# Kernel optimization log

Measured on AMD Instinct MI355X. Metric: run time of the kernel, lower is better.

## Reference

```python
import jax, jax.numpy as jnp
import numpy as np

WS = 8        # window_size
SHIFT = True
NHEADS = 4
DIM = 192

def _ln(x, g, b, eps=1e-5):
    mu = jnp.mean(x, axis=-1, keepdims=True)
    var = jnp.var(x, axis=-1, keepdims=True)
    return (x - mu) * jax.lax.rsqrt(var + eps) * g + b

def setup_inputs() -> dict:
    key = jax.random.key(0)
    ks = jax.random.split(key, 16)
    d = DIM
    s = 0.02
    return {
        "x":      jax.random.normal(ks[0], (4, d, 256, 256), jnp.float32),
        "g1":     jnp.ones((d,), jnp.float32),
        "b1":     jnp.zeros((d,), jnp.float32),
        "w_qkv":  jax.random.normal(ks[1], (d, 3 * d), jnp.float32) * s,
        "b_qkv":  jnp.zeros((3 * d,), jnp.float32),
        "w_o":    jax.random.normal(ks[2], (d, d), jnp.float32) * s,
        "b_o":    jnp.zeros((d,), jnp.float32),
        "g2":     jnp.ones((d,), jnp.float32),
        "b2":     jnp.zeros((d,), jnp.float32),
        "w_m1":   jax.random.normal(ks[3], (d, 4 * d), jnp.float32) * s,
        "b_m1":   jnp.zeros((4 * d,), jnp.float32),
        "w_m2":   jax.random.normal(ks[4], (4 * d, d), jnp.float32) * s,
        "b_m2":   jnp.zeros((d,), jnp.float32),
    }

def reference(x, g1, b1, w_qkv, b_qkv, w_o, b_o, g2, b2, w_m1, b_m1, w_m2, b_m2):
    B, C, H, W = x.shape
    pad_h = (-H) % WS
    pad_w = (-W) % WS
    x = jnp.pad(x, ((0, 0), (0, 0), (0, pad_h), (0, pad_w)))
    Hp, Wp = H + pad_h, W + pad_w
    if SHIFT:
        x = jnp.roll(x, (-(WS // 2), -(WS // 2)), axis=(2, 3))
    # window partition: (B,C,Hp,Wp) -> (nW, WS*WS, C)
    w = x.reshape(B, C, Hp // WS, WS, Wp // WS, WS)
    w = jnp.transpose(w, (0, 2, 4, 3, 5, 1)).reshape(-1, WS * WS, C)
    w = _ln(w, g1, b1)
    # multi-head self-attention (torch MHA: fused qkv proj, scale 1/sqrt(hd))
    qkv = w @ w_qkv + b_qkv                      # (nW, T, 3C)
    q, k, v = jnp.split(qkv, 3, axis=-1)
    hd = C // NHEADS
    def heads(t):
        return t.reshape(t.shape[0], t.shape[1], NHEADS, hd).transpose(0, 2, 1, 3)
    q, k, v = heads(q), heads(k), heads(v)
    scale = 1.0 / np.sqrt(hd).astype(np.float32)
    attn = jax.nn.softmax(jnp.einsum('nhqd,nhkd->nhqk', q * scale, k), axis=-1)
    o = jnp.einsum('nhqk,nhkd->nhqd', attn, v)
    o = o.transpose(0, 2, 1, 3).reshape(-1, WS * WS, C) @ w_o + b_o
    w = w + o
    h = _ln(w, g2, b2)
    w = w + (jax.nn.gelu(h @ w_m1 + b_m1, approximate=False) @ w_m2 + b_m2)
    # window reverse: (nW, WS*WS, C) -> (B,C,Hp,Wp)
    x = w.reshape(B, Hp // WS, Wp // WS, WS, WS, C)
    x = jnp.transpose(x, (0, 5, 1, 3, 2, 4)).reshape(B, C, Hp, Wp)
    if SHIFT:
        x = jnp.roll(x, (WS // 2, WS // 2), axis=(2, 3))
    return x[:, :, :H, :W]
```

## Files before the change

### kernel.cpp

```cpp
#include <hip/hip_runtime.h>
#include <hip/hip_bf16.h>
#include <cmath>


using bf16 = __hip_bfloat16;
typedef __attribute__((ext_vector_type(8))) short short8;
typedef __attribute__((ext_vector_type(4))) float f32x4;

__device__ __forceinline__ float b2f(bf16 v) { return __bfloat162float(v); }
__device__ __forceinline__ bf16  f2b(float v) { return __float2bfloat16(v); }

template <bool ISBF>
__device__ __forceinline__ float gldf(const void* p, size_t i) {
  if constexpr (ISBF) return b2f(((const bf16*)p)[i]);
  else                return ((const float*)p)[i];
}
template <bool ISBF>
__device__ __forceinline__ void gst(void* p, size_t i, float v) {
  if constexpr (ISBF) ((bf16*)p)[i] = f2b(v);
  else                ((float*)p)[i] = v;
}

template <bool ISBF>
__device__ __forceinline__ void transpose_body(
    const void* w_qkv, const void* w_o, const void* w_m1, const void* w_m2,
    bf16* ws, int id)
{
  if (id < 110592) {
    int n = id / 192, k = id - n * 192;
    ws[id] = f2b(gldf<ISBF>(w_qkv, (size_t)k * 576 + n));
  } else if (id < 147456) {
    int l = id - 110592;
    int n = l / 192, k = l - n * 192;
    ws[id] = f2b(gldf<ISBF>(w_o, (size_t)k * 192 + n));
  } else if (id < 294912) {
    int l = id - 147456;
    int n = l / 192, k = l - n * 192;
    ws[id] = f2b(gldf<ISBF>(w_m1, (size_t)k * 768 + n));
  } else {
    int l = id - 294912;
    int n = l / 768, k = l - n * 768;
    ws[id] = f2b(gldf<ISBF>(w_m2, (size_t)k * 192 + n));
  }
}

__global__ __launch_bounds__(256) void transpose_weights(
    const void* w_qkv, const void* w_o, const void* w_m1, const void* w_m2,
    bf16* ws, int isbf)
{
  int id = blockIdx.x * 256 + threadIdx.x;
  if (id >= 442368) return;
  if (isbf) transpose_body<true >(w_qkv, w_o, w_m1, w_m2, ws, id);
  else      transpose_body<false>(w_qkv, w_o, w_m1, w_m2, ws, id);
}

__device__ __forceinline__ void stage48(bf16* dst, const bf16* src, int tid) {
  for (int idx = tid; idx < 1152; idx += 256) {
    int r = idx / 24, g = idx - r * 24;
    *reinterpret_cast<short8*>(dst + r * 200 + g * 8) =
        *reinterpret_cast<const short8*>(src + r * 192 + g * 8);
  }
}
__device__ __forceinline__ void stage96(bf16* dst, const bf16* srcBase,
                                        int srcStride, int kOff, int tid) {
  for (int i = 0; i < 3; ++i) {
    int idx = tid + i * 256;
    int r = idx >> 3, g = idx & 7;
    short8 v = {0, 0, 0, 0, 0, 0, 0, 0};
    if (g < 6)
      v = *reinterpret_cast<const short8*>(srcBase + (size_t)r * srcStride +
                                           kOff + g * 8);
    *reinterpret_cast<short8*>(dst + r * 72 + g * 8) = v;
  }
}

template <int NT, int KS>
__device__ __forceinline__ void gemm_tile(const bf16* sA, int lda,
                                          const bf16* sB, int ldb,
                                          f32x4* c, int w, int col, int quad) {
  const bf16* ap = sA + (w * 16 + col) * lda + quad * 8;
#pragma unroll
  for (int ks = 0; ks < KS; ++ks) {
    short8 a = *reinterpret_cast<const short8*>(ap + ks * 32);
#pragma unroll
    for (int nt = 0; nt < NT; ++nt) {
      short8 b = *reinterpret_cast<const short8*>(
          sB + (nt * 16 + col) * ldb + ks * 32 + quad * 8);
      c[nt] = __builtin_amdgcn_mfma_f32_16x16x32_bf16(a, b, c[nt], 0, 0, 0);
    }
  }
}

template <bool ISBF>
__device__ void swin_mfma_body(
    const void* __restrict__ x,
    const void* __restrict__ g1, const void* __restrict__ b1,
    const void* __restrict__ b_qkv, const void* __restrict__ b_o,
    const void* __restrict__ g2, const void* __restrict__ b2,
    const void* __restrict__ b_m1, const void* __restrict__ b_m2,
    const bf16* __restrict__ ws, void* __restrict__ out, char* smem)
{
  bf16* sX = reinterpret_cast<bf16*>(smem);
  bf16* sW = reinterpret_cast<bf16*>(smem + 25600);
  bf16* sQ = reinterpret_cast<bf16*>(smem + 44800);
  bf16* sK = reinterpret_cast<bf16*>(smem + 54016);
  bf16* sV = reinterpret_cast<bf16*>(smem + 63232);
  bf16* sP = reinterpret_cast<bf16*>(smem + 70144);
  float* red = reinterpret_cast<float*>(smem + 70144);

  const bf16* wsq  = ws;
  const bf16* wso  = ws + 110592;
  const bf16* wsm1 = ws + 147456;
  const bf16* wsm2 = ws + 294912;

  const int wi = blockIdx.x;
  const int bb = wi >> 10, hy = (wi >> 5) & 31, wx = wi & 31;
  const int tid = threadIdx.x;
  const int w = tid >> 6, lane = tid & 63, col = lane & 15, quad = lane >> 4;
  const int t = tid >> 2, qq = tid & 3;
  const int ty = t >> 3, tx = t & 7;
  const int ph = (hy * 8 + ty + 4) & 255;
  const int pw = (wx * 8 + tx + 4) & 255;

  {
    int buf = tid >> 7, rh = tid & 127, row = rh >> 1, half = rh & 1;
    short8 z = {0, 0, 0, 0, 0, 0, 0, 0};
    *reinterpret_cast<short8*>((buf ? sK : sQ) + row * 72 + 48 + half * 8) = z;
  }

  {
    const size_t xb = (((size_t)(bb * 192 + qq * 48)) << 16) + (ph << 8) + pw;
    float s = 0.f, ss = 0.f;
    for (int j = 0; j < 48; ++j) {
      float v = gldf<ISBF>(x, xb + ((size_t)j << 16));
      s += v; ss += v * v;
      sX[t * 200 + qq * 48 + j] = f2b(v);
    }
    red[(t * 4 + qq) * 2 + 0] = s;
    red[(t * 4 + qq) * 2 + 1] = ss;
  }
  __syncthreads();
  {
    float s = 0.f, ss = 0.f;
    for (int k = 0; k < 4; ++k) {
      s  += red[(t * 4 + k) * 2 + 0];
      ss += red[(t * 4 + k) * 2 + 1];
    }
    float mu  = s * (1.f / 192.f);
    float var = ss * (1.f / 192.f) - mu * mu;
    float inv = rsqrtf(var + 1e-5f);
    for (int j = 0; j < 48; ++j) {
      int c = qq * 48 + j;
      float v = b2f(sX[t * 200 + c]);
      sX[t * 200 + c] =
          f2b((v - mu) * inv * gldf<ISBF>(g1, c) + gldf<ISBF>(b1, c));
    }
  }

  f32x4 accW[12];
#pragma unroll
  for (int i = 0; i < 12; ++i) accW[i] = {0.f, 0.f, 0.f, 0.f};
  const float scale = 0.14433756729740643f;

  for (int h = 0; h < 4; ++h) {
    __syncthreads();
    stage48(sW, wsq + (size_t)(h * 48) * 192, tid);
    __syncthreads();
    {
      f32x4 c3[3] = {{0,0,0,0},{0,0,0,0},{0,0,0,0}};
      gemm_tile<3, 6>(sX, 200, sW, 200, c3, w, col, quad);
#pragma unroll
      for (int nt = 0; nt < 3; ++nt) {
        float bq = gldf<ISBF>(b_qkv, h * 48 + nt * 16 + col);
#pragma unroll
        for (int r = 0; r < 4; ++r)
          sQ[(w * 16 + quad * 4 + r) * 72 + nt * 16 + col] =
              f2b((c3[nt][r] + bq) * scale);
      }
    }
    __syncthreads();
    stage48(sW, wsq + (size_t)(192 + h * 48) * 192, tid);
    __syncthreads();
    {
      f32x4 c3[3] = {{0,0,0,0},{0,0,0,0},{0,0,0,0}};
      gemm_tile<3, 6>(sX, 200, sW, 200, c3, w, col, quad);
#pragma unroll
      for (int nt = 0; nt < 3; ++nt) {
        float bk = gldf<ISBF>(b_qkv, 192 + h * 48 + nt * 16 + col);
#pragma unroll
        for (int r = 0; r < 4; ++r)
          sK[(w * 16 + quad * 4 + r) * 72 + nt * 16 + col] = f2b(c3[nt][r] + bk);
      }
    }
    __syncthreads();
    stage48(sW, wsq + (size_t)(384 + h * 48) * 192, tid);
    __syncthreads();
    {
      f32x4 c3[3] = {{0,0,0,0},{0,0,0,0},{0,0,0,0}};
      gemm_tile<3, 6>(sX, 200, sW, 200, c3, w, col, quad);
#pragma unroll
      for (int nt = 0; nt < 3; ++nt) {
        float bv = gldf<ISBF>(b_qkv, 384 + h * 48 + nt * 16 + col);
#pragma unroll
        for (int r = 0; r < 4; ++r)
          sV[(nt * 16 + col) * 72 + w * 16 + quad * 4 + r] = f2b(c3[nt][r] + bv);
      }
    }
    __syncthreads();

    {
      f32x4 s4[4] = {{0,0,0,0},{0,0,0,0},{0,0,0,0},{0,0,0,0}};
      gemm_tile<4, 2>(sQ, 72, sK, 72, s4, w, col, quad);
      float inv[4];
#pragma unroll
      for (int r = 0; r < 4; ++r) {
        float m = fmaxf(fmaxf(s4[0][r], s4[1][r]), fmaxf(s4[2][r], s4[3][r]));
#pragma unroll
        for (int msk = 1; msk < 16; msk <<= 1) m = fmaxf(m, __shfl_xor(m, msk, 64));
        float sum = 0.f;
#pragma unroll
        for (int nt = 0; nt < 4; ++nt) {
          float e = expf(s4[nt][r] - m);
          s4[nt][r] = e; sum += e;
        }
#pragma unroll
        for (int msk = 1; msk < 16; msk <<= 1) sum += __shfl_xor(sum, msk, 64);
        inv[r] = 1.f / sum;
      }
#pragma unroll
      for (int nt = 0; nt < 4; ++nt)
#pragma unroll
        for (int r = 0; r < 4; ++r)
          sP[(w * 16 + quad * 4 + r) * 72 + nt * 16 + col] =
              f2b(s4[nt][r] * inv[r]);
    }
    {
      f32x4 c3[3] = {{0,0,0,0},{0,0,0,0},{0,0,0,0}};
      gemm_tile<3, 2>(sP, 72, sV, 72, c3, w, col, quad);
#pragma unroll
      for (int nt = 0; nt < 3; ++nt)
#pragma unroll
        for (int r = 0; r < 4; ++r)
          sQ[(w * 16 + quad * 4 + r) * 72 + nt * 16 + col] = f2b(c3[nt][r]);
    }
    for (int s = 0; s < 2; ++s) {
      __syncthreads();
      stage96(sW, wso + (size_t)(s * 96) * 192, 192, h * 48, tid);
      __syncthreads();
      gemm_tile<6, 2>(sQ, 72, sW, 72, accW + s * 6, w, col, quad);
    }
  }

  {
#pragma unroll
    for (int nt = 0; nt < 12; ++nt) {
      int c = nt * 16 + col;
      float bo = gldf<ISBF>(b_o, c);
#pragma unroll
      for (int r = 0; r < 4; ++r)
        accW[nt][r] += bo + b2f(sX[(w * 16 + quad * 4 + r) * 200 + c]);
    }
    float su[4] = {0,0,0,0}, sq[4] = {0,0,0,0};
#pragma unroll
    for (int nt = 0; nt < 12; ++nt)
#pragma unroll
      for (int r = 0; r < 4; ++r) {
        su[r] += accW[nt][r]; sq[r] += accW[nt][r] * accW[nt][r];
      }
#pragma unroll
    for (int r = 0; r < 4; ++r) {
#pragma unroll
      for (int msk = 1; msk < 16; msk <<= 1) {
        su[r] += __shfl_xor(su[r], msk, 64);
        sq[r] += __shfl_xor(sq[r], msk, 64);
      }
    }
    float mu[4], inv[4];
#pragma unroll
    for (int r = 0; r < 4; ++r) {
      mu[r] = su[r] * (1.f / 192.f);
      inv[r] = rsqrtf(sq[r] * (1.f / 192.f) - mu[r] * mu[r] + 1e-5f);
    }
#pragma unroll
    for (int nt = 0; nt < 12; ++nt) {
      int c = nt * 16 + col;
      float g2c = gldf<ISBF>(g2, c), b2c = gldf<ISBF>(b2, c);
      float bm2 = gldf<ISBF>(b_m2, c);
#pragma unroll
      for (int r = 0; r < 4; ++r) {
        float hv = (accW[nt][r] - mu[r]) * inv[r] * g2c + b2c;
        sX[(w * 16 + quad * 4 + r) * 200 + c] = f2b(hv);
        accW[nt][r] += bm2;
      }
    }
  }

  for (int ch = 0; ch < 16; ++ch) {
    __syncthreads();
    stage48(sW, wsm1 + (size_t)(ch * 48) * 192, tid);
    __syncthreads();
    {
      f32x4 c3[3] = {{0,0,0,0},{0,0,0,0},{0,0,0,0}};
      gemm_tile<3, 6>(sX, 200, sW, 200, c3, w, col, quad);
#pragma unroll
      for (int nt = 0; nt < 3; ++nt) {
        float bm1 = gldf<ISBF>(b_m1, ch * 48 + nt * 16 + col);
#pragma unroll
        for (int r = 0; r < 4; ++r) {
          float v = c3[nt][r] + bm1;
          v = 0.5f * v * (1.f + erff(v * 0.70710678118654752f));
          sK[(w * 16 + quad * 4 + r) * 72 + nt * 16 + col] = f2b(v);
        }
      }
    }
    for (int s = 0; s < 2; ++s) {
      __syncthreads();
      stage96(sW, wsm2 + (size_t)(s * 96) * 768, 768, ch * 48, tid);
      __syncthreads();
      gemm_tile<6, 2>(sK, 72, sW, 72, accW + s * 6, w, col, quad);
    }
  }

  __syncthreads();
#pragma unroll
  for (int nt = 0; nt < 12; ++nt)
#pragma unroll
    for (int r = 0; r < 4; ++r)
      sX[(w * 16 + quad * 4 + r) * 200 + nt * 16 + col] = f2b(accW[nt][r]);
  __syncthreads();
  {
    const size_t ob = (((size_t)(bb * 192 + qq * 48)) << 16) + (ph << 8) + pw;
    for (int j = 0; j < 48; ++j)
      gst<ISBF>(out, ob + ((size_t)j << 16), b2f(sX[t * 200 + qq * 48 + j]));
  }
}

__global__ __launch_bounds__(256, 2) void swin_mfma(
    const void* x, const void* g1, const void* b1, const void* b_qkv,
    const void* b_o, const void* g2, const void* b2, const void* b_m1,
    const void* b_m2, const bf16* ws, void* out, int isbf)
{
  __shared__ __align__(16) char smem[79360];
  if (isbf)
    swin_mfma_body<true >(x, g1, b1, b_qkv, b_o, g2, b2, b_m1, b_m2, ws, out, smem);
  else
    swin_mfma_body<false>(x, g1, b1, b_qkv, b_o, g2, b2, b_m1, b_m2, ws, out, smem);
}

template <bool ISBF>
__device__ __forceinline__ void gld4(const void* p, size_t i, float* o) {
  if constexpr (ISBF) {
    uint2 u = *reinterpret_cast<const uint2*>((const bf16*)p + i);
    union { unsigned int b; float f; } a;
    a.b = u.x << 16;          o[0] = a.f;
    a.b = u.x & 0xffff0000u;  o[1] = a.f;
    a.b = u.y << 16;          o[2] = a.f;
    a.b = u.y & 0xffff0000u;  o[3] = a.f;
  } else {
    float4 f = *reinterpret_cast<const float4*>((const float*)p + i);
    o[0] = f.x; o[1] = f.y; o[2] = f.z; o[3] = f.w;
  }
}

template <bool ISBF>
__device__ void swin_scalar_body(
    const void* x, const void* g1, const void* b1, const void* w_qkv,
    const void* b_qkv, const void* w_o, const void* b_o, const void* g2,
    const void* b2, const void* w_m1, const void* b_m1, const void* w_m2,
    const void* b_m2, void* out, bf16* s_w, char* s_buf)
{
  bf16*  sQ  = reinterpret_cast<bf16*>(s_buf);
  bf16*  sK  = reinterpret_cast<bf16*>(s_buf + 6400);
  bf16*  sV  = reinterpret_cast<bf16*>(s_buf + 12800);
  float* sS  = reinterpret_cast<float*>(s_buf + 19200);
  bf16*  sO  = sQ;
  bf16*  sH  = reinterpret_cast<bf16*>(s_buf);
  bf16*  sC  = reinterpret_cast<bf16*>(s_buf + 25600);
  float* red1 = reinterpret_cast<float*>(s_buf);
  float* red2 = reinterpret_cast<float*>(s_buf + 25600);

  const int wi = blockIdx.x;
  const int bb = wi >> 10, hy = (wi >> 5) & 31, wx = wi & 31;
  const int tid = threadIdx.x;
  const int t = tid >> 2, q = tid & 3;
  const int ty = t >> 3, tx = t & 7;
  const int ph = (hy * 8 + ty + 4) & 255, pw = (wx * 8 + tx + 4) & 255;
  float acc[48];
  {
    const size_t xb = (((size_t)(bb * 192 + q * 48)) << 16) + (ph << 8) + pw;
    float s = 0.f, ss = 0.f;
    for (int j = 0; j < 48; ++j) {
      float v = gldf<ISBF>(x, xb + ((size_t)j << 16));
      s += v; ss += v * v;
      s_w[t * 200 + q * 48 + j] = f2b(v);
    }
    red1[(t * 4 + q) * 2 + 0] = s; red1[(t * 4 + q) * 2 + 1] = ss;
  }
  __syncthreads();
  {
    float s = 0.f, ss = 0.f;
    for (int k = 0; k < 4; ++k) { s += red1[(t*4+k)*2]; ss += red1[(t*4+k)*2+1]; }
    float mu = s / 192.f, var = ss / 192.f - mu * mu, inv = rsqrtf(var + 1e-5f);
    for (int j = 0; j < 48; ++j) {
      int c = q * 48 + j;
      float v = (b2f(s_w[t*200+c]) - mu) * inv * gldf<ISBF>(g1,c) + gldf<ISBF>(b1,c);
      s_w[t * 200 + c] = f2b(v);
      acc[j] = v;
    }
  }
  __syncthreads();
  const float scale = 0.14433756729740643f;
  for (int h = 0; h < 4; ++h) {
    {
      float aq[12], ak[12], av[12];
      for (int j = 0; j < 12; ++j) {
        aq[j] = gldf<ISBF>(b_qkv, h*48 + q*12 + j);
        ak[j] = gldf<ISBF>(b_qkv, 192 + h*48 + q*12 + j);
        av[j] = gldf<ISBF>(b_qkv, 384 + h*48 + q*12 + j);
      }
      for (int c = 0; c < 192; ++c) {
        float a = b2f(s_w[t * 200 + c]);
        const size_t wr = (size_t)c * 576 + h * 48 + q * 12;
        float wv[4];
        for (int j0 = 0; j0 < 12; j0 += 4) {
          gld4<ISBF>(w_qkv, wr + j0, wv);
          for (int k = 0; k < 4; ++k) aq[j0+k] += a * wv[k];
        }
        for (int j0 = 0; j0 < 12; j0 += 4) {
          gld4<ISBF>(w_qkv, wr + 192 + j0, wv);
          for (int k = 0; k < 4; ++k) ak[j0+k] += a * wv[k];
        }
        for (int j0 = 0; j0 < 12; j0 += 4) {
          gld4<ISBF>(w_qkv, wr + 384 + j0, wv);
          for (int k = 0; k < 4; ++k) av[j0+k] += a * wv[k];
        }
      }
      for (int j = 0; j < 12; ++j) {
        sQ[t*50 + q*12 + j] = f2b(aq[j] * scale);
        sK[t*50 + q*12 + j] = f2b(ak[j]);
        sV[t*50 + q*12 + j] = f2b(av[j]);
      }
    }
    __syncthreads();
    {
      float as[16];
      for (int j = 0; j < 16; ++j) as[j] = 0.f;
      for (int d = 0; d < 48; ++d) {
        float qv = b2f(sQ[t*50 + d]);
        for (int j = 0; j < 16; ++j) as[j] += qv * b2f(sK[(q*16+j)*50 + d]);
      }
      for (int j = 0; j < 16; ++j) sS[t*66 + q*16 + j] = as[j];
    }
    __syncthreads();
    if (tid < 64) {
      float mx = -1e30f;
      for (int j = 0; j < 64; ++j) mx = fmaxf(mx, sS[tid*66+j]);
      float sum = 0.f;
      for (int j = 0; j < 64; ++j) { float e = expf(sS[tid*66+j]-mx); sS[tid*66+j]=e; sum+=e; }
      float r = 1.f / sum;
      for (int j = 0; j < 64; ++j) sS[tid*66+j] *= r;
    }
    __syncthreads();
    {
      float ao[12];
      for (int j = 0; j < 12; ++j) ao[j] = 0.f;
      for (int j = 0; j < 64; ++j) {
        float p = sS[t*66 + j];
        for (int k = 0; k < 12; ++k) ao[k] += p * b2f(sV[j*50 + q*12 + k]);
      }
      for (int j = 0; j < 12; ++j) sO[t*50 + q*12 + j] = f2b(ao[j]);
    }
    __syncthreads();
    for (int d = 0; d < 48; ++d) {
      float ov = b2f(sO[t*50 + d]);
      const size_t wr = (size_t)(h*48+d) * 192 + q * 48;
      float wv[4];
      for (int j0 = 0; j0 < 48; j0 += 4) {
        gld4<ISBF>(w_o, wr + j0, wv);
        for (int k = 0; k < 4; ++k) acc[j0+k] += ov * wv[k];
      }
    }
    __syncthreads();
  }
  for (int j = 0; j < 48; ++j) acc[j] += gldf<ISBF>(b_o, q*48 + j);
  {
    float s = 0.f, ss = 0.f;
    for (int j = 0; j < 48; ++j) { s += acc[j]; ss += acc[j]*acc[j]; }
    red2[(t*4+q)*2] = s; red2[(t*4+q)*2+1] = ss;
  }
  __syncthreads();
  {
    float s = 0.f, ss = 0.f;
    for (int k = 0; k < 4; ++k) { s += red2[(t*4+k)*2]; ss += red2[(t*4+k)*2+1]; }
    float mu = s/192.f, var = ss/192.f - mu*mu, inv = rsqrtf(var + 1e-5f);
    for (int j = 0; j < 48; ++j) {
      int c = q*48 + j;
      sH[t*200+c] = f2b((acc[j]-mu)*inv*gldf<ISBF>(g2,c) + gldf<ISBF>(b2,c));
    }
  }
  for (int j = 0; j < 48; ++j) acc[j] += gldf<ISBF>(b_m2, q*48 + j);
  __syncthreads();
  for (int ch = 0; ch < 8; ++ch) {
    float am[24];
    for (int j = 0; j < 24; ++j) am[j] = gldf<ISBF>(b_m1, ch*96 + q*24 + j);
    for (int c = 0; c < 192; ++c) {
      float hv = b2f(sH[t*200 + c]);
      const size_t wr = (size_t)c * 768 + ch*96 + q*24;
      float wv[4];
      for (int j0 = 0; j0 < 24; j0 += 4) {
        gld4<ISBF>(w_m1, wr + j0, wv);
        for (int k = 0; k < 4; ++k) am[j0+k] += hv * wv[k];
      }
    }
    for (int j = 0; j < 24; ++j) {
      float v = am[j];
      am[j] = 0.5f * v * (1.f + erff(v * 0.70710678118654752f));
    }
    for (int j = 0; j < 24; ++j) sC[t*104 + q*24 + j] = f2b(am[j]);
    __syncthreads();
    for (int u = 0; u < 96; ++u) {
      float hv = b2f(sC[t*104 + u]);
      const size_t wr = (size_t)(ch*96+u) * 192 + q*48;
      float wv[4];
      for (int j0 = 0; j0 < 48; j0 += 4) {
        gld4<ISBF>(w_m2, wr + j0, wv);
        for (int k = 0; k < 4; ++k) acc[j0+k] += hv * wv[k];
      }
    }
    __syncthreads();
  }
  {
    const size_t ob = (((size_t)(bb*192 + q*48)) << 16) + (ph << 8) + pw;
    for (int j = 0; j < 48; ++j) gst<ISBF>(out, ob + ((size_t)j << 16), acc[j]);
  }
}

__global__ __launch_bounds__(256) void swin_scalar(
    const void* x, const void* g1, const void* b1, const void* w_qkv,
    const void* b_qkv, const void* w_o, const void* b_o, const void* g2,
    const void* b2, const void* w_m1, const void* b_m1, const void* w_m2,
    const void* b_m2, void* out, int isbf)
{
  __shared__ bf16 s_w[64 * 200];
  __shared__ __align__(16) char s_buf[38912];
  if (isbf)
    swin_scalar_body<true >(x,g1,b1,w_qkv,b_qkv,w_o,b_o,g2,b2,w_m1,b_m1,w_m2,b_m2,out,s_w,s_buf);
  else
    swin_scalar_body<false>(x,g1,b1,w_qkv,b_qkv,w_o,b_o,g2,b2,w_m1,b_m1,w_m2,b_m2,out,s_w,s_buf);
}

extern "C" void kernel_launch(void* const* d_in, const int* in_sizes, int n_in,
                              void* d_out, int out_size, void* d_ws, size_t ws_size,
                              hipStream_t stream) {
  const int isbf = (n_in > 1 && in_sizes != nullptr && in_sizes[1] == 384) ? 1 : 0;
  if (ws_size >= 884736) {
    transpose_weights<<<dim3(1728), dim3(256), 0, stream>>>(
        d_in[3], d_in[5], d_in[9], d_in[11], (bf16*)d_ws, isbf);
    swin_mfma<<<dim3(4096), dim3(256), 0, stream>>>(
        d_in[0], d_in[1], d_in[2], d_in[4], d_in[6], d_in[7], d_in[8],
        d_in[10], d_in[12], (const bf16*)d_ws, d_out, isbf);
  } else {
    swin_scalar<<<dim3(4096), dim3(256), 0, stream>>>(
        d_in[0], d_in[1], d_in[2], d_in[3], d_in[4], d_in[5], d_in[6],
        d_in[7], d_in[8], d_in[9], d_in[10], d_in[11], d_in[12], d_out, isbf);
  }
}
```

Baseline: 1.470 ms.

## Read MFMA weight fragments directly from global memory instead of LDS staging

Drops the stage48/stage96 LDS staging of weight tiles. Each GEMM now loads its B fragments straight from the pre-transposed global weight buffer, which should be cache-resident. This removes many block-wide barriers and LDS copies, and shrinks shared memory from about 79KB to 60KB. In exchange, each of the four waves fetches the same weight fragments separately from global memory, so MFMA issue is exposed to L1/L2 latency and extra cache traffic.

```diff
diff --git a/kernel.cpp b/kernel.cpp
--- a/kernel.cpp
+++ b/kernel.cpp
@@ -54,26 +54,6 @@
   else      transpose_body<false>(w_qkv, w_o, w_m1, w_m2, ws, id);
 }
 
-__device__ __forceinline__ void stage48(bf16* dst, const bf16* src, int tid) {
-  for (int idx = tid; idx < 1152; idx += 256) {
-    int r = idx / 24, g = idx - r * 24;
-    *reinterpret_cast<short8*>(dst + r * 200 + g * 8) =
-        *reinterpret_cast<const short8*>(src + r * 192 + g * 8);
-  }
-}
-__device__ __forceinline__ void stage96(bf16* dst, const bf16* srcBase,
-                                        int srcStride, int kOff, int tid) {
-  for (int i = 0; i < 3; ++i) {
-    int idx = tid + i * 256;
-    int r = idx >> 3, g = idx & 7;
-    short8 v = {0, 0, 0, 0, 0, 0, 0, 0};
-    if (g < 6)
-      v = *reinterpret_cast<const short8*>(srcBase + (size_t)r * srcStride +
-                                           kOff + g * 8);
-    *reinterpret_cast<short8*>(dst + r * 72 + g * 8) = v;
-  }
-}
-
 template <int NT, int KS>
 __device__ __forceinline__ void gemm_tile(const bf16* sA, int lda,
                                           const bf16* sB, int ldb,
@@ -86,6 +66,40 @@
     for (int nt = 0; nt < NT; ++nt) {
       short8 b = *reinterpret_cast<const short8*>(
           sB + (nt * 16 + col) * ldb + ks * 32 + quad * 8);
+      c[nt] = __builtin_amdgcn_mfma_f32_16x16x32_bf16(a, b, c[nt], 0, 0, 0);
+    }
+  }
+}
+
+template <int NT, int KS>
+__device__ __forceinline__ void gemm_gB(const bf16* sA, int lda,
+    const bf16* __restrict__ gB, int ldk, f32x4* c, int w, int col, int quad) {
+  const bf16* ap = sA + (w * 16 + col) * lda + quad * 8;
+  const bf16* bp = gB + col * ldk + quad * 8;
+#pragma unroll
+  for (int ks = 0; ks < KS; ++ks) {
+    short8 a = *reinterpret_cast<const short8*>(ap + ks * 32);
+#pragma unroll
+    for (int nt = 0; nt < NT; ++nt) {
+      short8 b = *reinterpret_cast<const short8*>(bp + nt * 16 * ldk + ks * 32);
+      c[nt] = __builtin_amdgcn_mfma_f32_16x16x32_bf16(a, b, c[nt], 0, 0, 0);
+    }
+  }
+}
+
+template <int NT>
+__device__ __forceinline__ void gemm_gB_p48(const bf16* sA, int lda,
+    const bf16* __restrict__ gB, int ldk, f32x4* c, int w, int col, int quad) {
+  const bf16* ap = sA + (w * 16 + col) * lda + quad * 8;
+  const bf16* bp = gB + col * ldk + quad * 8;
+#pragma unroll
+  for (int ks = 0; ks < 2; ++ks) {
+    short8 a = *reinterpret_cast<const short8*>(ap + ks * 32);
+#pragma unroll
+    for (int nt = 0; nt < NT; ++nt) {
+      short8 b = {0, 0, 0, 0, 0, 0, 0, 0};
+      if (ks == 0 || quad < 2)
+        b = *reinterpret_cast<const short8*>(bp + nt * 16 * ldk + ks * 32);
       c[nt] = __builtin_amdgcn_mfma_f32_16x16x32_bf16(a, b, c[nt], 0, 0, 0);
     }
   }
@@ -101,12 +115,11 @@
     const bf16* __restrict__ ws, void* __restrict__ out, char* smem)
 {
   bf16* sX = reinterpret_cast<bf16*>(smem);
-  bf16* sW = reinterpret_cast<bf16*>(smem + 25600);
-  bf16* sQ = reinterpret_cast<bf16*>(smem + 44800);
-  bf16* sK = reinterpret_cast<bf16*>(smem + 54016);
-  bf16* sV = reinterpret_cast<bf16*>(smem + 63232);
-  bf16* sP = reinterpret_cast<bf16*>(smem + 70144);
-  float* red = reinterpret_cast<float*>(smem + 70144);
+  bf16* sQ = reinterpret_cast<bf16*>(smem + 25600);
+  bf16* sK = reinterpret_cast<bf16*>(smem + 34816);
+  bf16* sV = reinterpret_cast<bf16*>(smem + 44032);
+  bf16* sP = reinterpret_cast<bf16*>(smem + 50944);
+  float* red = reinterpret_cast<float*>(smem + 50944);
 
   const bf16* wsq  = ws;
   const bf16* wso  = ws + 110592;
@@ -156,6 +169,7 @@
           f2b((v - mu) * inv * gldf<ISBF>(g1, c) + gldf<ISBF>(b1, c));
     }
   }
+  __syncthreads();
 
   f32x4 accW[12];
 #pragma unroll
@@ -163,12 +177,10 @@
   const float scale = 0.14433756729740643f;
 
   for (int h = 0; h < 4; ++h) {
-    __syncthreads();
-    stage48(sW, wsq + (size_t)(h * 48) * 192, tid);
-    __syncthreads();
+    if (h) __syncthreads();
     {
       f32x4 c3[3] = {{0,0,0,0},{0,0,0,0},{0,0,0,0}};
-      gemm_tile<3, 6>(sX, 200, sW, 200, c3, w, col, quad);
+      gemm_gB<3, 6>(sX, 200, wsq + (size_t)(h * 48) * 192, 192, c3, w, col, quad);
 #pragma unroll
       for (int nt = 0; nt < 3; ++nt) {
         float bq = gldf<ISBF>(b_qkv, h * 48 + nt * 16 + col);
@@ -178,12 +190,9 @@
               f2b((c3[nt][r] + bq) * scale);
       }
     }
-    __syncthreads();
-    stage48(sW, wsq + (size_t)(192 + h * 48) * 192, tid);
-    __syncthreads();
     {
       f32x4 c3[3] = {{0,0,0,0},{0,0,0,0},{0,0,0,0}};
-      gemm_tile<3, 6>(sX, 200, sW, 200, c3, w, col, quad);
+      gemm_gB<3, 6>(sX, 200, wsq + (size_t)(192 + h * 48) * 192, 192, c3, w, col, quad);
 #pragma unroll
       for (int nt = 0; nt < 3; ++nt) {
         float bk = gldf<ISBF>(b_qkv, 192 + h * 48 + nt * 16 + col);
@@ -192,12 +201,9 @@
           sK[(w * 16 + quad * 4 + r) * 72 + nt * 16 + col] = f2b(c3[nt][r] + bk);
       }
     }
-    __syncthreads();
-    stage48(sW, wsq + (size_t)(384 + h * 48) * 192, tid);
-    __syncthreads();
     {
       f32x4 c3[3] = {{0,0,0,0},{0,0,0,0},{0,0,0,0}};
-      gemm_tile<3, 6>(sX, 200, sW, 200, c3, w, col, quad);
+      gemm_gB<3, 6>(sX, 200, wsq + (size_t)(384 + h * 48) * 192, 192, c3, w, col, quad);
 #pragma unroll
       for (int nt = 0; nt < 3; ++nt) {
         float bv = gldf<ISBF>(b_qkv, 384 + h * 48 + nt * 16 + col);
@@ -234,6 +240,8 @@
           sP[(w * 16 + quad * 4 + r) * 72 + nt * 16 + col] =
               f2b(s4[nt][r] * inv[r]);
     }
+    __syncthreads();
+
     {
       f32x4 c3[3] = {{0,0,0,0},{0,0,0,0},{0,0,0,0}};
       gemm_tile<3, 2>(sP, 72, sV, 72, c3, w, col, quad);
@@ -243,13 +251,14 @@
         for (int r = 0; r < 4; ++r)
           sQ[(w * 16 + quad * 4 + r) * 72 + nt * 16 + col] = f2b(c3[nt][r]);
     }
-    for (int s = 0; s < 2; ++s) {
-      __syncthreads();
-      stage96(sW, wso + (size_t)(s * 96) * 192, 192, h * 48, tid);
-      __syncthreads();
-      gemm_tile<6, 2>(sQ, 72, sW, 72, accW + s * 6, w, col, quad);
-    }
-  }
+    __syncthreads();
+
+    gemm_gB_p48<6>(sQ, 72, wso + (size_t)(0 * 96) * 192 + h * 48, 192,
+                   accW + 0, w, col, quad);
+    gemm_gB_p48<6>(sQ, 72, wso + (size_t)(1 * 96) * 192 + h * 48, 192,
+                   accW + 6, w, col, quad);
+  }
+  __syncthreads();
 
   {
 #pragma unroll
@@ -294,14 +303,12 @@
       }
     }
   }
+  __syncthreads();
 
   for (int ch = 0; ch < 16; ++ch) {
-    __syncthreads();
-    stage48(sW, wsm1 + (size_t)(ch * 48) * 192, tid);
-    __syncthreads();
     {
       f32x4 c3[3] = {{0,0,0,0},{0,0,0,0},{0,0,0,0}};
-      gemm_tile<3, 6>(sX, 200, sW, 200, c3, w, col, quad);
+      gemm_gB<3, 6>(sX, 200, wsm1 + (size_t)(ch * 48) * 192, 192, c3, w, col, quad);
 #pragma unroll
       for (int nt = 0; nt < 3; ++nt) {
         float bm1 = gldf<ISBF>(b_m1, ch * 48 + nt * 16 + col);
@@ -313,12 +320,11 @@
         }
       }
     }
-    for (int s = 0; s < 2; ++s) {
-      __syncthreads();
-      stage96(sW, wsm2 + (size_t)(s * 96) * 768, 768, ch * 48, tid);
-      __syncthreads();
-      gemm_tile<6, 2>(sK, 72, sW, 72, accW + s * 6, w, col, quad);
-    }
+    __syncthreads();
+    gemm_gB_p48<6>(sK, 72, wsm2 + (size_t)(0 * 96) * 768 + ch * 48, 768,
+                   accW + 0, w, col, quad);
+    gemm_gB_p48<6>(sK, 72, wsm2 + (size_t)(1 * 96) * 768 + ch * 48, 768,
+                   accW + 6, w, col, quad);
   }
 
   __syncthreads();
@@ -340,7 +346,7 @@
     const void* b_o, const void* g2, const void* b2, const void* b_m1,
     const void* b_m2, const bf16* ws, void* out, int isbf)
 {
-  __shared__ __align__(16) char smem[79360];
+  __shared__ __align__(16) char smem[60160];
   if (isbf)
     swin_mfma_body<true >(x, g1, b1, b_qkv, b_o, g2, b2, b_m1, b_m2, ws, out, smem);
   else
```

Measured after the change: 2.158 ms. 1.47x slower.

## Process two windows per block sharing staged weight tiles in LDS

Applied to the files above, without the earlier changes.

Each 512-thread block now handles two windows. One shared weight staging buffer serves both windows, and each window keeps its own activation, Q/K/V and P buffers. The aim is to halve the global-to-LDS weight traffic per window and the number of staging passes. In exchange LDS use per block grows to about 122KB, so only one block fits per CU, and barriers now synchronize all 512 threads.

```diff
diff --git a/kernel.cpp b/kernel.cpp
--- a/kernel.cpp
+++ b/kernel.cpp
@@ -54,23 +54,27 @@
   else      transpose_body<false>(w_qkv, w_o, w_m1, w_m2, ws, id);
 }
 
-__device__ __forceinline__ void stage48(bf16* dst, const bf16* src, int tid) {
-  for (int idx = tid; idx < 1152; idx += 256) {
+__device__ __forceinline__ void stage48_512(bf16* dst, const bf16* src,
+                                            int tid512) {
+  for (int idx = tid512; idx < 1152; idx += 512) {
     int r = idx / 24, g = idx - r * 24;
     *reinterpret_cast<short8*>(dst + r * 200 + g * 8) =
         *reinterpret_cast<const short8*>(src + r * 192 + g * 8);
   }
 }
-__device__ __forceinline__ void stage96(bf16* dst, const bf16* srcBase,
-                                        int srcStride, int kOff, int tid) {
-  for (int i = 0; i < 3; ++i) {
-    int idx = tid + i * 256;
-    int r = idx >> 3, g = idx & 7;
-    short8 v = {0, 0, 0, 0, 0, 0, 0, 0};
-    if (g < 6)
-      v = *reinterpret_cast<const short8*>(srcBase + (size_t)r * srcStride +
-                                           kOff + g * 8);
-    *reinterpret_cast<short8*>(dst + r * 72 + g * 8) = v;
+__device__ __forceinline__ void stage96_512(bf16* dst, const bf16* srcBase,
+                                            int srcStride, int kOff,
+                                            int tid512) {
+  for (int i = 0; i < 2; ++i) {
+    int idx = tid512 + i * 512;
+    if (idx < 768) {
+      int r = idx >> 3, g = idx & 7;
+      short8 v = {0, 0, 0, 0, 0, 0, 0, 0};
+      if (g < 6)
+        v = *reinterpret_cast<const short8*>(srcBase + (size_t)r * srcStride +
+                                             kOff + g * 8);
+      *reinterpret_cast<short8*>(dst + r * 72 + g * 8) = v;
+    }
   }
 }
 
@@ -100,22 +104,25 @@
     const void* __restrict__ b_m1, const void* __restrict__ b_m2,
     const bf16* __restrict__ ws, void* __restrict__ out, char* smem)
 {
-  bf16* sX = reinterpret_cast<bf16*>(smem);
-  bf16* sW = reinterpret_cast<bf16*>(smem + 25600);
-  bf16* sQ = reinterpret_cast<bf16*>(smem + 44800);
-  bf16* sK = reinterpret_cast<bf16*>(smem + 54016);
-  bf16* sV = reinterpret_cast<bf16*>(smem + 63232);
-  bf16* sP = reinterpret_cast<bf16*>(smem + 70144);
-  float* red = reinterpret_cast<float*>(smem + 70144);
+  const int tid512 = threadIdx.x;
+  const int wsel   = tid512 >> 8;
+  const int tid    = tid512 & 255;
+
+  bf16* sW  = reinterpret_cast<bf16*>(smem);
+  bf16* sP  = reinterpret_cast<bf16*>(smem + wsel * 9216);
+  bf16* sX  = reinterpret_cast<bf16*>(smem + 19200 + wsel * 25600);
+  bf16* sQ  = reinterpret_cast<bf16*>(smem + 70400 + wsel * 9216);
+  bf16* sK  = reinterpret_cast<bf16*>(smem + 88832 + wsel * 9216);
+  bf16* sV  = reinterpret_cast<bf16*>(smem + 107264 + wsel * 6912);
+  float* red = reinterpret_cast<float*>(smem + 121088 + wsel * 2048);
 
   const bf16* wsq  = ws;
   const bf16* wso  = ws + 110592;
   const bf16* wsm1 = ws + 147456;
   const bf16* wsm2 = ws + 294912;
 
-  const int wi = blockIdx.x;
+  const int wi = blockIdx.x * 2 + wsel;
   const int bb = wi >> 10, hy = (wi >> 5) & 31, wx = wi & 31;
-  const int tid = threadIdx.x;
   const int w = tid >> 6, lane = tid & 63, col = lane & 15, quad = lane >> 4;
   const int t = tid >> 2, qq = tid & 3;
   const int ty = t >> 3, tx = t & 7;
@@ -164,7 +171,7 @@
 
   for (int h = 0; h < 4; ++h) {
     __syncthreads();
-    stage48(sW, wsq + (size_t)(h * 48) * 192, tid);
+    stage48_512(sW, wsq + (size_t)(h * 48) * 192, tid512);
     __syncthreads();
     {
       f32x4 c3[3] = {{0,0,0,0},{0,0,0,0},{0,0,0,0}};
@@ -179,7 +186,7 @@
       }
     }
     __syncthreads();
-    stage48(sW, wsq + (size_t)(192 + h * 48) * 192, tid);
+    stage48_512(sW, wsq + (size_t)(192 + h * 48) * 192, tid512);
     __syncthreads();
     {
       f32x4 c3[3] = {{0,0,0,0},{0,0,0,0},{0,0,0,0}};
@@ -193,7 +200,7 @@
       }
     }
     __syncthreads();
-    stage48(sW, wsq + (size_t)(384 + h * 48) * 192, tid);
+    stage48_512(sW, wsq + (size_t)(384 + h * 48) * 192, tid512);
     __syncthreads();
     {
       f32x4 c3[3] = {{0,0,0,0},{0,0,0,0},{0,0,0,0}};
@@ -245,7 +252,7 @@
     }
     for (int s = 0; s < 2; ++s) {
       __syncthreads();
-      stage96(sW, wso + (size_t)(s * 96) * 192, 192, h * 48, tid);
+      stage96_512(sW, wso + (size_t)(s * 96) * 192, 192, h * 48, tid512);
       __syncthreads();
       gemm_tile<6, 2>(sQ, 72, sW, 72, accW + s * 6, w, col, quad);
     }
@@ -297,7 +304,7 @@
 
   for (int ch = 0; ch < 16; ++ch) {
     __syncthreads();
-    stage48(sW, wsm1 + (size_t)(ch * 48) * 192, tid);
+    stage48_512(sW, wsm1 + (size_t)(ch * 48) * 192, tid512);
     __syncthreads();
     {
       f32x4 c3[3] = {{0,0,0,0},{0,0,0,0},{0,0,0,0}};
@@ -315,7 +322,7 @@
     }
     for (int s = 0; s < 2; ++s) {
       __syncthreads();
-      stage96(sW, wsm2 + (size_t)(s * 96) * 768, 768, ch * 48, tid);
+      stage96_512(sW, wsm2 + (size_t)(s * 96) * 768, 768, ch * 48, tid512);
       __syncthreads();
       gemm_tile<6, 2>(sK, 72, sW, 72, accW + s * 6, w, col, quad);
     }
@@ -335,12 +342,12 @@
   }
 }
 
-__global__ __launch_bounds__(256, 2) void swin_mfma(
+__global__ __launch_bounds__(512, 1) void swin_mfma(
     const void* x, const void* g1, const void* b1, const void* b_qkv,
     const void* b_o, const void* g2, const void* b2, const void* b_m1,
     const void* b_m2, const bf16* ws, void* out, int isbf)
 {
-  __shared__ __align__(16) char smem[79360];
+  __shared__ __align__(16) char smem[125184];
   if (isbf)
     swin_mfma_body<true >(x, g1, b1, b_qkv, b_o, g2, b2, b_m1, b_m2, ws, out, smem);
   else
@@ -556,7 +563,7 @@
   if (ws_size >= 884736) {
     transpose_weights<<<dim3(1728), dim3(256), 0, stream>>>(
         d_in[3], d_in[5], d_in[9], d_in[11], (bf16*)d_ws, isbf);
-    swin_mfma<<<dim3(4096), dim3(256), 0, stream>>>(
+    swin_mfma<<<dim3(2048), dim3(512), 0, stream>>>(
         d_in[0], d_in[1], d_in[2], d_in[4], d_in[6], d_in[7], d_in[8],
         d_in[10], d_in[12], (const bf16*)d_ws, d_out, isbf);
   } else {
```

New measurement: 1.441 ms. -2.0%, faster.
